# Performance work log

Measured on AMD Instinct MI355X. Metric: run time of the kernel, lower is better.

Reference implementation:

```python
import jax, jax.numpy as jnp
import numpy as np
import math

B, S, N, D, H = 4, 64, 256, 512, 8
DEPTH = D // H

def setup_inputs() -> dict:
    key = jax.random.key(0)
    ks = jax.random.split(key, 9)
    scale = 1.0 / math.sqrt(D)
    return {
        "x": jax.random.normal(ks[0], (B, S, N, D), dtype=jnp.float32),
        "Wq": jax.random.normal(ks[1], (D, D), dtype=jnp.float32) * scale,
        "bq": jax.random.normal(ks[2], (D,), dtype=jnp.float32) * 0.01,
        "Wk": jax.random.normal(ks[3], (D, D), dtype=jnp.float32) * scale,
        "bk": jax.random.normal(ks[4], (D,), dtype=jnp.float32) * 0.01,
        "Wv": jax.random.normal(ks[5], (D, D), dtype=jnp.float32) * scale,
        "bv": jax.random.normal(ks[6], (D,), dtype=jnp.float32) * 0.01,
        "Wo": jax.random.normal(ks[7], (D, D), dtype=jnp.float32) * scale,
        "bo": jax.random.normal(ks[8], (D,), dtype=jnp.float32) * 0.01,
    }

def _split_heads(t):
    # (B, S, M, D) -> (B, H, S, M, depth); matches split_head.forward (4D path)
    # followed by the att_dim==2 permute(0, 2, 1, 3, 4) in cross_attention.
    b, s, m, _ = t.shape
    return t.reshape(b, s, m, H, DEPTH).transpose(0, 3, 1, 2, 4)

def reference(x, Wq, bq, Wk, bk, Wv, bv, Wo, bo):
    b, s, n, d = x.shape
    # att_dim == 2: query is the cls token along the joint/patch axis.
    q = _split_heads(x[:, :, 0:1, :] @ Wq + bq)   # (B, H, S, 1, depth)
    k = _split_heads(x @ Wk + bk)                  # (B, H, S, N, depth)
    v = _split_heads(x @ Wv + bv)                  # (B, H, S, N, depth)
    # scaled dot product attention (mask is None in cross_attention)
    logits = jnp.einsum('bhsqd,bhskd->bhsqk', q, k) / math.sqrt(DEPTH)
    attn = jax.nn.softmax(logits, axis=-1)         # (B, H, S, 1, N)
    ctx = jnp.einsum('bhsqk,bhskd->bhsqd', attn, v)  # (B, H, S, 1, depth)
    # permute(0, 2, 3, 1, 4) then reshape (B, S, 1, D)
    concat = ctx.transpose(0, 2, 3, 1, 4).reshape(b, s, 1, d)
    return concat @ Wo + bo
```

## Files before the change

### kernel.cpp

```cpp
#include <hip/hip_runtime.h>
#include <stdint.h>
#include <math.h>


__device__ __forceinline__ void gemm_ks_body(
    const float* __restrict__ A, long a_row_stride, int a_col_off_mult,
    const float* __restrict__ W, const float* __restrict__ bias,
    float* __restrict__ C, int rt, int jt, int t,
    float (*a_s)[512], float (*red_s)[4][64]) {
  const int w = t >> 6, lane = t & 63;

#pragma unroll
  for (int l = 0; l < 2; ++l) {
    int flat4 = t + l * 256;
    int arow = flat4 >> 7;
    int k4 = (flat4 & 127) * 4;
    float4 v = *(const float4*)&A[(long)(rt * 4 + arow) * a_row_stride +
                                  (long)jt * a_col_off_mult + k4];
    a_s[arow][k4] = v.x; a_s[arow][k4 + 1] = v.y;
    a_s[arow][k4 + 2] = v.z; a_s[arow][k4 + 3] = v.w;
  }
  __syncthreads();

  const int j = jt * 64 + lane;
  float acc0 = 0.f, acc1 = 0.f, acc2 = 0.f, acc3 = 0.f;
  const float* wp = W + (long)(w * 128) * 512 + j;
  const float* ap = &a_s[0][w * 128];
#pragma unroll 8
  for (int k = 0; k < 128; ++k) {
    float wv = wp[(long)k * 512];
    acc0 += ap[k] * wv;
    acc1 += ap[512 + k] * wv;
    acc2 += ap[1024 + k] * wv;
    acc3 += ap[1536 + k] * wv;
  }
  if (w > 0) {
    red_s[w - 1][0][lane] = acc0;
    red_s[w - 1][1][lane] = acc1;
    red_s[w - 1][2][lane] = acc2;
    red_s[w - 1][3][lane] = acc3;
  }
  __syncthreads();
  if (w == 0) {
#pragma unroll
    for (int rr = 0; rr < 3; ++rr) {
      acc0 += red_s[rr][0][lane];
      acc1 += red_s[rr][1][lane];
      acc2 += red_s[rr][2][lane];
      acc3 += red_s[rr][3][lane];
    }
    const float b = bias[j];
    C[(long)(rt * 4 + 0) * 512 + j] = acc0 + b;
    C[(long)(rt * 4 + 1) * 512 + j] = acc1 + b;
    C[(long)(rt * 4 + 2) * 512 + j] = acc2 + b;
    C[(long)(rt * 4 + 3) * 512 + j] = acc3 + b;
  }
}

__global__ __launch_bounds__(256) void prep_kernel(
    const float* __restrict__ x, const float* __restrict__ Wq,
    const float* __restrict__ bq, const float* __restrict__ Wk,
    float* __restrict__ WkT, float* __restrict__ q) {
  __shared__ float a_s[4][512];
  __shared__ float red_s[3][4][64];
  const int t = threadIdx.x;

  if (blockIdx.x < 256) {
    float (*tile)[64] = (float(*)[64])&a_s[0][0];
    const int j0 = (blockIdx.x & 15) * 32;
    const int c0 = (blockIdx.x >> 4) * 32;
    {
      const int row = t >> 3;
      const int c4 = (t & 7) * 4;
      float4 v = *(const float4*)&Wk[(long)(j0 + row) * 512 + c0 + c4];
      float* tr = &tile[0][0] + row * 33;
      tr[c4] = v.x; tr[c4 + 1] = v.y; tr[c4 + 2] = v.z; tr[c4 + 3] = v.w;
    }
    __syncthreads();
    {
      const int row = t >> 3;
      const int j4 = (t & 7) * 4;
      const float* tb = &tile[0][0];
      float4 v = make_float4(tb[j4 * 33 + row], tb[(j4 + 1) * 33 + row],
                             tb[(j4 + 2) * 33 + row], tb[(j4 + 3) * 33 + row]);
      *(float4*)&WkT[(long)(c0 + row) * 512 + j0 + j4] = v;
    }
  } else {
    const int bid = blockIdx.x - 256;
    const int rt = bid & 63;
    const int jt = bid >> 6;
    gemm_ks_body(x, 131072L, 0, Wq, bq, q, rt, jt, t, a_s, red_s);
  }
}

__global__ __launch_bounds__(256) void gemm_ks_kernel(
    const float* __restrict__ A, long a_row_stride, int a_col_off_mult,
    const float* __restrict__ W, const float* __restrict__ bias,
    float* __restrict__ C) {
  __shared__ float a_s[4][512];
  __shared__ float red_s[3][4][64];
  gemm_ks_body(A, a_row_stride, a_col_off_mult, W, bias, C,
               blockIdx.x, blockIdx.y, threadIdx.x, a_s, red_s);
}

__global__ __launch_bounds__(256) void r_kernel(
    const float* __restrict__ q, const float* __restrict__ WkT,
    float* __restrict__ r_all) {
  const int rt = blockIdx.x;
  const int h = blockIdx.y;
  const int t = threadIdx.x;
  __shared__ float q_s[4][64];

  {
    int row = t >> 6, c = t & 63;
    q_s[row][c] = q[(long)(rt * 4 + row) * 512 + h * 64 + c];
  }
  __syncthreads();

  const int jp4 = (t & 127) * 4;
  const int rh = t >> 7;
  float4 acc0 = make_float4(0.f, 0.f, 0.f, 0.f);
  float4 acc1 = make_float4(0.f, 0.f, 0.f, 0.f);
#pragma unroll 8
  for (int c = 0; c < 64; ++c) {
    float4 w4 = *(const float4*)&WkT[(long)(h * 64 + c) * 512 + jp4];
    float q0 = q_s[rh * 2][c], q1 = q_s[rh * 2 + 1][c];
    acc0.x += q0 * w4.x; acc0.y += q0 * w4.y; acc0.z += q0 * w4.z; acc0.w += q0 * w4.w;
    acc1.x += q1 * w4.x; acc1.y += q1 * w4.y; acc1.z += q1 * w4.z; acc1.w += q1 * w4.w;
  }
  *(float4*)&r_all[(long)(rt * 4 + rh * 2) * 4096 + h * 512 + jp4] = acc0;
  *(float4*)&r_all[(long)(rt * 4 + rh * 2 + 1) * 4096 + h * 512 + jp4] = acc1;
}

__global__ __launch_bounds__(1024) void attn_kernel(
    const float* __restrict__ x, const float* __restrict__ r_all,
    float* __restrict__ Y) {
  const int bs = blockIdx.x;
  const int t = threadIdx.x;
  const int w = t >> 6, lane = t & 63;
  const float* xb = x + (long)bs * 131072;
  __shared__ float p_s[8][256];
  __shared__ float yp[8][512];

  const int hg = w & 1;
  const int rw = w >> 1;

  float rv[4][8];
  const float* rb = r_all + (long)bs * 4096 + lane * 8;
#pragma unroll
  for (int hi = 0; hi < 4; ++hi) {
    const int h = hg * 4 + hi;
    float4 a = *(const float4*)&rb[h * 512];
    float4 b = *(const float4*)&rb[h * 512 + 4];
    rv[hi][0] = a.x; rv[hi][1] = a.y; rv[hi][2] = a.z; rv[hi][3] = a.w;
    rv[hi][4] = b.x; rv[hi][5] = b.y; rv[hi][6] = b.z; rv[hi][7] = b.w;
  }

#pragma unroll 4
  for (int i = 0; i < 32; ++i) {
    const int n = rw * 32 + i;
    const float* xr = xb + (long)n * 512 + lane * 8;
    float4 xa = *(const float4*)xr;
    float4 xb4 = *(const float4*)(xr + 4);
    float acc[4];
#pragma unroll
    for (int hi = 0; hi < 4; ++hi)
      acc[hi] = xa.x * rv[hi][0] + xa.y * rv[hi][1] + xa.z * rv[hi][2] + xa.w * rv[hi][3]
              + xb4.x * rv[hi][4] + xb4.y * rv[hi][5] + xb4.z * rv[hi][6] + xb4.w * rv[hi][7];
#pragma unroll
    for (int j = 0; j < 2; ++j) {
      float v = (lane & 2) ? acc[j] : acc[j + 2];
      float tt = __shfl_xor(v, 2);
      acc[j] = ((lane & 2) ? acc[j + 2] : acc[j]) + tt;
    }
    {
      float v = (lane & 1) ? acc[0] : acc[1];
      float tt = __shfl_xor(v, 1);
      acc[0] = ((lane & 1) ? acc[1] : acc[0]) + tt;
    }
    acc[0] += __shfl_xor(acc[0], 4);
    acc[0] += __shfl_xor(acc[0], 8);
    acc[0] += __shfl_xor(acc[0], 16);
    acc[0] += __shfl_xor(acc[0], 32);
    if (lane < 4) p_s[hg * 4 + lane][n] = acc[0] * 0.125f;
  }
  __syncthreads();

  if (w < 8) {
    float4 lv = *(const float4*)&p_s[w][lane * 4];
    float m = fmaxf(fmaxf(lv.x, lv.y), fmaxf(lv.z, lv.w));
    for (int o = 32; o; o >>= 1) m = fmaxf(m, __shfl_xor(m, o));
    float e0 = __expf(lv.x - m), e1 = __expf(lv.y - m);
    float e2 = __expf(lv.z - m), e3 = __expf(lv.w - m);
    float s = e0 + e1 + e2 + e3;
    for (int o = 32; o; o >>= 1) s += __shfl_xor(s, o);
    const float inv = 1.f / s;
    *(float4*)&p_s[w][lane * 4] = make_float4(e0 * inv, e1 * inv, e2 * inv, e3 * inv);
  }
  __syncthreads();

  const int d = t & 511;
  const int half = t >> 9;
  float acc[8] = {};
  const float* xb2 = xb + ((long)half * 128) * 512 + d;
#pragma unroll 8
  for (int n = 0; n < 128; ++n) {
    float xv = xb2[(long)n * 512];
#pragma unroll
    for (int h = 0; h < 8; ++h)
      acc[h] += p_s[h][half * 128 + n] * xv;
  }
  if (half == 1) {
#pragma unroll
    for (int h = 0; h < 8; ++h) yp[h][d] = acc[h];
  }
  __syncthreads();
  if (half == 0) {
#pragma unroll
    for (int h = 0; h < 8; ++h)
      Y[(long)bs * 4096 + h * 512 + d] = acc[h] + yp[h][d];
  }
}

extern "C" void kernel_launch(void* const* d_in, const int* in_sizes, int n_in,
                              void* d_out, int out_size, void* d_ws, size_t ws_size,
                              hipStream_t stream) {
  (void)in_sizes; (void)n_in; (void)out_size; (void)ws_size;
  const float* x  = (const float*)d_in[0];
  const float* Wq = (const float*)d_in[1];
  const float* bq = (const float*)d_in[2];
  const float* Wk = (const float*)d_in[3];
  const float* bk = (const float*)d_in[4];  (void)bk;
  const float* Wv = (const float*)d_in[5];
  const float* bv = (const float*)d_in[6];
  const float* Wo = (const float*)d_in[7];
  const float* bo = (const float*)d_in[8];
  float* out = (float*)d_out;

  float* WkT = (float*)d_ws;
  float* q   = WkT + 262144;
  float* r   = q + 131072;
  float* Y   = r + 1048576;
  float* ctx = Y + 1048576;

  prep_kernel<<<768, 256, 0, stream>>>(x, Wq, bq, Wk, WkT, q);
  r_kernel<<<dim3(64, 8), 256, 0, stream>>>(q, WkT, r);
  attn_kernel<<<256, 1024, 0, stream>>>(x, r, Y);
  gemm_ks_kernel<<<dim3(64, 8), 256, 0, stream>>>(Y, 4096L, 512, Wv, bv, ctx);
  gemm_ks_kernel<<<dim3(64, 8), 256, 0, stream>>>(ctx, 512L, 0, Wo, bo, out);
}
```

Measured before the change: 264.7 us.

## Fuse r=q·Wk^T projection into attention kernel and batch x row loads

Removes the Wk transpose pass and the separate r_kernel; each attention block now computes its own r vectors (q times Wk rows per head) into shared memory before scoring. The scoring loop is restructured to issue eight rows of x loads up front before reducing, to raise memory-level parallelism. This cuts two launches and the r_all round trip through global memory, at the cost of each of 256 blocks re-reading all of Wk (1 MB, likely L2-resident) and higher register pressure from the batched loads.

After: 317.9 us. 1.2x slower.

```diff
diff --git a/kernel.cpp b/kernel.cpp
--- a/kernel.cpp
+++ b/kernel.cpp
@@ -57,42 +57,6 @@
   }
 }
 
-__global__ __launch_bounds__(256) void prep_kernel(
-    const float* __restrict__ x, const float* __restrict__ Wq,
-    const float* __restrict__ bq, const float* __restrict__ Wk,
-    float* __restrict__ WkT, float* __restrict__ q) {
-  __shared__ float a_s[4][512];
-  __shared__ float red_s[3][4][64];
-  const int t = threadIdx.x;
-
-  if (blockIdx.x < 256) {
-    float (*tile)[64] = (float(*)[64])&a_s[0][0];
-    const int j0 = (blockIdx.x & 15) * 32;
-    const int c0 = (blockIdx.x >> 4) * 32;
-    {
-      const int row = t >> 3;
-      const int c4 = (t & 7) * 4;
-      float4 v = *(const float4*)&Wk[(long)(j0 + row) * 512 + c0 + c4];
-      float* tr = &tile[0][0] + row * 33;
-      tr[c4] = v.x; tr[c4 + 1] = v.y; tr[c4 + 2] = v.z; tr[c4 + 3] = v.w;
-    }
-    __syncthreads();
-    {
-      const int row = t >> 3;
-      const int j4 = (t & 7) * 4;
-      const float* tb = &tile[0][0];
-      float4 v = make_float4(tb[j4 * 33 + row], tb[(j4 + 1) * 33 + row],
-                             tb[(j4 + 2) * 33 + row], tb[(j4 + 3) * 33 + row]);
-      *(float4*)&WkT[(long)(c0 + row) * 512 + j0 + j4] = v;
-    }
-  } else {
-    const int bid = blockIdx.x - 256;
-    const int rt = bid & 63;
-    const int jt = bid >> 6;
-    gemm_ks_body(x, 131072L, 0, Wq, bq, q, rt, jt, t, a_s, red_s);
-  }
-}
-
 __global__ __launch_bounds__(256) void gemm_ks_kernel(
     const float* __restrict__ A, long a_row_stride, int a_col_off_mult,
     const float* __restrict__ W, const float* __restrict__ bias,
@@ -103,86 +67,94 @@
                blockIdx.x, blockIdx.y, threadIdx.x, a_s, red_s);
 }
 
-__global__ __launch_bounds__(256) void r_kernel(
-    const float* __restrict__ q, const float* __restrict__ WkT,
-    float* __restrict__ r_all) {
-  const int rt = blockIdx.x;
-  const int h = blockIdx.y;
-  const int t = threadIdx.x;
-  __shared__ float q_s[4][64];
-
+__device__ __forceinline__ void row_reduce(
+    const float4 xa, const float4 xb4, const float rv[4][8],
+    int lane, int hg, float (*p_s)[256], int n) {
+  float acc[4];
+#pragma unroll
+  for (int hi = 0; hi < 4; ++hi)
+    acc[hi] = xa.x * rv[hi][0] + xa.y * rv[hi][1] + xa.z * rv[hi][2] + xa.w * rv[hi][3]
+            + xb4.x * rv[hi][4] + xb4.y * rv[hi][5] + xb4.z * rv[hi][6] + xb4.w * rv[hi][7];
+#pragma unroll
+  for (int j = 0; j < 2; ++j) {
+    float v = (lane & 2) ? acc[j] : acc[j + 2];
+    float tt = __shfl_xor(v, 2);
+    acc[j] = ((lane & 2) ? acc[j + 2] : acc[j]) + tt;
+  }
   {
-    int row = t >> 6, c = t & 63;
-    q_s[row][c] = q[(long)(rt * 4 + row) * 512 + h * 64 + c];
-  }
-  __syncthreads();
-
-  const int jp4 = (t & 127) * 4;
-  const int rh = t >> 7;
-  float4 acc0 = make_float4(0.f, 0.f, 0.f, 0.f);
-  float4 acc1 = make_float4(0.f, 0.f, 0.f, 0.f);
-#pragma unroll 8
-  for (int c = 0; c < 64; ++c) {
-    float4 w4 = *(const float4*)&WkT[(long)(h * 64 + c) * 512 + jp4];
-    float q0 = q_s[rh * 2][c], q1 = q_s[rh * 2 + 1][c];
-    acc0.x += q0 * w4.x; acc0.y += q0 * w4.y; acc0.z += q0 * w4.z; acc0.w += q0 * w4.w;
-    acc1.x += q1 * w4.x; acc1.y += q1 * w4.y; acc1.z += q1 * w4.z; acc1.w += q1 * w4.w;
-  }
-  *(float4*)&r_all[(long)(rt * 4 + rh * 2) * 4096 + h * 512 + jp4] = acc0;
-  *(float4*)&r_all[(long)(rt * 4 + rh * 2 + 1) * 4096 + h * 512 + jp4] = acc1;
-}
-
-__global__ __launch_bounds__(1024) void attn_kernel(
-    const float* __restrict__ x, const float* __restrict__ r_all,
-    float* __restrict__ Y) {
+    float v = (lane & 1) ? acc[0] : acc[1];
+    float tt = __shfl_xor(v, 1);
+    acc[0] = ((lane & 1) ? acc[1] : acc[0]) + tt;
+  }
+  acc[0] += __shfl_xor(acc[0], 4);
+  acc[0] += __shfl_xor(acc[0], 8);
+  acc[0] += __shfl_xor(acc[0], 16);
+  acc[0] += __shfl_xor(acc[0], 32);
+  if (lane < 4) p_s[hg * 4 + lane][n] = acc[0] * 0.125f;
+}
+
+__global__ __launch_bounds__(1024, 4) void attn_kernel(
+    const float* __restrict__ x, const float* __restrict__ q_all,
+    const float* __restrict__ Wk, float* __restrict__ Y) {
   const int bs = blockIdx.x;
   const int t = threadIdx.x;
   const int w = t >> 6, lane = t & 63;
   const float* xb = x + (long)bs * 131072;
+  __shared__ float r_s[4096];
   __shared__ float p_s[8][256];
   __shared__ float yp[8][512];
 
   const int hg = w & 1;
   const int rw = w >> 1;
 
+  {
+    const int d = t >> 1, hh = t & 1;
+    const float* wrow = Wk + (long)d * 512 + hh * 256;
+    const float* qp = q_all + (long)bs * 512 + hh * 256;
+#pragma unroll
+    for (int hi = 0; hi < 4; ++hi) {
+      float racc = 0.f;
+#pragma unroll
+      for (int c4 = 0; c4 < 16; ++c4) {
+        float4 wv = *(const float4*)&wrow[hi * 64 + c4 * 4];
+        float4 qv = *(const float4*)&qp[hi * 64 + c4 * 4];
+        racc += qv.x * wv.x + qv.y * wv.y + qv.z * wv.z + qv.w * wv.w;
+      }
+      r_s[(hh * 4 + hi) * 512 + d] = racc;
+    }
+  }
+  __syncthreads();
+
   float rv[4][8];
-  const float* rb = r_all + (long)bs * 4096 + lane * 8;
 #pragma unroll
   for (int hi = 0; hi < 4; ++hi) {
     const int h = hg * 4 + hi;
-    float4 a = *(const float4*)&rb[h * 512];
-    float4 b = *(const float4*)&rb[h * 512 + 4];
+    float4 a = *(const float4*)&r_s[h * 512 + lane * 8];
+    float4 b = *(const float4*)&r_s[h * 512 + lane * 8 + 4];
     rv[hi][0] = a.x; rv[hi][1] = a.y; rv[hi][2] = a.z; rv[hi][3] = a.w;
     rv[hi][4] = b.x; rv[hi][5] = b.y; rv[hi][6] = b.z; rv[hi][7] = b.w;
   }
 
-#pragma unroll 4
-  for (int i = 0; i < 32; ++i) {
-    const int n = rw * 32 + i;
-    const float* xr = xb + (long)n * 512 + lane * 8;
-    float4 xa = *(const float4*)xr;
-    float4 xb4 = *(const float4*)(xr + 4);
-    float acc[4];
-#pragma unroll
-    for (int hi = 0; hi < 4; ++hi)
-      acc[hi] = xa.x * rv[hi][0] + xa.y * rv[hi][1] + xa.z * rv[hi][2] + xa.w * rv[hi][3]
-              + xb4.x * rv[hi][4] + xb4.y * rv[hi][5] + xb4.z * rv[hi][6] + xb4.w * rv[hi][7];
-#pragma unroll
-    for (int j = 0; j < 2; ++j) {
-      float v = (lane & 2) ? acc[j] : acc[j + 2];
-      float tt = __shfl_xor(v, 2);
-      acc[j] = ((lane & 2) ? acc[j + 2] : acc[j]) + tt;
-    }
-    {
-      float v = (lane & 1) ? acc[0] : acc[1];
-      float tt = __shfl_xor(v, 1);
-      acc[0] = ((lane & 1) ? acc[1] : acc[0]) + tt;
-    }
-    acc[0] += __shfl_xor(acc[0], 4);
-    acc[0] += __shfl_xor(acc[0], 8);
-    acc[0] += __shfl_xor(acc[0], 16);
-    acc[0] += __shfl_xor(acc[0], 32);
-    if (lane < 4) p_s[hg * 4 + lane][n] = acc[0] * 0.125f;
+#pragma unroll
+  for (int ib = 0; ib < 4; ++ib) {
+    const int n0 = rw * 32 + ib * 8;
+    const float* xr = xb + (long)n0 * 512 + lane * 8;
+    float4 a0 = *(const float4*)(xr +    0), b0 = *(const float4*)(xr +    4);
+    float4 a1 = *(const float4*)(xr +  512), b1 = *(const float4*)(xr +  516);
+    float4 a2 = *(const float4*)(xr + 1024), b2 = *(const float4*)(xr + 1028);
+    float4 a3 = *(const float4*)(xr + 1536), b3 = *(const float4*)(xr + 1540);
+    float4 a4 = *(const float4*)(xr + 2048), b4 = *(const float4*)(xr + 2052);
+    float4 a5 = *(const float4*)(xr + 2560), b5 = *(const float4*)(xr + 2564);
+    float4 a6 = *(const float4*)(xr + 3072), b6 = *(const float4*)(xr + 3076);
+    float4 a7 = *(const float4*)(xr + 3584), b7 = *(const float4*)(xr + 3588);
+    row_reduce(a0, b0, rv, lane, hg, p_s, n0 + 0);
+    row_reduce(a1, b1, rv, lane, hg, p_s, n0 + 1);
+    row_reduce(a2, b2, rv, lane, hg, p_s, n0 + 2);
+    row_reduce(a3, b3, rv, lane, hg, p_s, n0 + 3);
+    row_reduce(a4, b4, rv, lane, hg, p_s, n0 + 4);
+    row_reduce(a5, b5, rv, lane, hg, p_s, n0 + 5);
+    row_reduce(a6, b6, rv, lane, hg, p_s, n0 + 6);
+    row_reduce(a7, b7, rv, lane, hg, p_s, n0 + 7);
   }
   __syncthreads();
 
@@ -237,15 +209,12 @@
   const float* bo = (const float*)d_in[8];
   float* out = (float*)d_out;
 
-  float* WkT = (float*)d_ws;
-  float* q   = WkT + 262144;
-  float* r   = q + 131072;
-  float* Y   = r + 1048576;
-  float* ctx = Y + 1048576;
-
-  prep_kernel<<<768, 256, 0, stream>>>(x, Wq, bq, Wk, WkT, q);
-  r_kernel<<<dim3(64, 8), 256, 0, stream>>>(q, WkT, r);
-  attn_kernel<<<256, 1024, 0, stream>>>(x, r, Y);
+  float* q_ws = (float*)d_ws;
+  float* Y    = q_ws + 131072;
+  float* ctx  = Y + 1048576;
+
+  gemm_ks_kernel<<<dim3(64, 8), 256, 0, stream>>>(x, 131072L, 0, Wq, bq, q_ws);
+  attn_kernel<<<256, 1024, 0, stream>>>(x, q_ws, Wk, Y);
   gemm_ks_kernel<<<dim3(64, 8), 256, 0, stream>>>(Y, 4096L, 512, Wv, bv, ctx);
   gemm_ks_kernel<<<dim3(64, 8), 256, 0, stream>>>(ctx, 512L, 0, Wo, bo, out);
 }
```
